# Performance work log

Hardware: AMD Instinct MI355X
Metric: run time of the kernel (lower is better)

## Reference

```python
import jax, jax.numpy as jnp
import numpy as np
from jax import lax

B, S, I, H, O, L = 32, 512, 256, 1024, 256, 3


def setup_inputs() -> dict:
    key = jax.random.key(0)
    ks = jax.random.split(key, 10)
    sc = 0.02
    return {
        "x": jax.random.normal(ks[0], (B, S, I), dtype=jnp.float32),
        "h0": jnp.zeros((B, L, H), dtype=jnp.float32),
        # layer 0 params: gates ordered [z, r, g]
        "Wx0": jax.random.normal(ks[1], (3, H, I), dtype=jnp.float32) * sc,
        "Wh0": jax.random.normal(ks[2], (3, H, H), dtype=jnp.float32) * sc,
        "bh0": jax.random.normal(ks[3], (3, H), dtype=jnp.float32) * sc,
        # layers 1..L-1 params (input dim = H)
        "Wx": jax.random.normal(ks[4], (L - 1, 3, H, H), dtype=jnp.float32) * sc,
        "Wh": jax.random.normal(ks[5], (L - 1, 3, H, H), dtype=jnp.float32) * sc,
        "bh": jax.random.normal(ks[6], (L - 1, 3, H), dtype=jnp.float32) * sc,
        "Wout": jax.random.normal(ks[7], (O, H), dtype=jnp.float32) * sc,
        "bout": jax.random.normal(ks[8], (O,), dtype=jnp.float32) * sc,
    }


def _gru_layer(x_seq, h0, Wx, Wh, bh):
    # x_seq: [S,B,Iin], h0: [B,H], Wx: [3,H,Iin], Wh: [3,H,H], bh: [3,H]
    # Precompute all input projections once (fused GEMM over full sequence).
    xproj = jnp.einsum('sbi,ghi->sbgh', x_seq, Wx)  # [S,B,3,H]

    def step(h, xp):
        z = jax.nn.sigmoid(xp[:, 0] + h @ Wh[0].T + bh[0])
        r = jax.nn.sigmoid(xp[:, 1] + h @ Wh[1].T + bh[1])
        g = jnp.tanh(xp[:, 2] + (r * h) @ Wh[2].T + bh[2])
        h_new = z * h + (1.0 - z) * g
        return h_new, h_new

    h_last, hs = lax.scan(step, h0, xproj)
    return hs, h_last  # hs: [S,B,H]


def reference(x, h0, Wx0, Wh0, bh0, Wx, Wh, bh, Wout, bout):
    seq = jnp.transpose(x, (1, 0, 2))  # [S,B,I]
    cur, hl = _gru_layer(seq, h0[:, 0], Wx0, Wh0, bh0)
    finals = [hl]
    n_extra = Wx.shape[0]
    for i in range(n_extra):  # small fixed layer count
        cur, hl = _gru_layer(cur, h0[:, i + 1], Wx[i], Wh[i], bh[i])
        finals.append(hl)
    out = cur @ Wout.T + bout  # [S,B,O]
    layer_output = jnp.transpose(out, (1, 0, 2))  # [B,S,O]
    hidden_state = jnp.stack(finals, axis=1)  # [B,L,H]
    return layer_output, hidden_state
```

## Files before the change

kernel.cpp:

```cpp
#include <hip/hip_runtime.h>
#include <cstdint>
#include <cstddef>

#define S_  512
#define H_  1024
#define H3  3072
#define OUT_OFF 4194304

typedef __attribute__((ext_vector_type(8))) short  short8;
typedef __attribute__((ext_vector_type(4))) float  f32x4;
typedef __attribute__((ext_vector_type(4))) unsigned short us4;
typedef __attribute__((ext_vector_type(4))) unsigned int   u32x4;
typedef unsigned long long u64;

#define MFMA __builtin_amdgcn_mfma_f32_16x16x32_bf16

static const size_t XP_OFF    = 0;
static const size_t H2_OFF    = 100663296;
static const size_t XBF_OFF   = 134217728;
static const size_t WX0B_OFF  = 142606336;
static const size_t WZR0_OFF  = 144179200;
static const size_t WG0_OFF   = 148373504;
static const size_t WZR1_OFF  = 150470656;
static const size_t WGX1_OFF  = 158859264;
static const size_t WG1_OFF   = 160956416;
static const size_t WZR2_OFF  = 163053568;
static const size_t WGX2_OFF  = 171442176;
static const size_t WG2_OFF   = 173539328;
static const size_t WOUTB_OFF = 175636480;
static const size_t ZBU_OFF   = 176160768;
static const size_t GXB_OFF   = 176553984;
static const size_t HROW_OFF  = 176947200;
static const size_t FLAG_OFF  = 177340416;
static const size_t HH_OFF    = 177344512;
static const size_t RHH_OFF   = 278597632;
static const size_t WS_HIST   = 379654144;
static const size_t WS_BASE   = 177737728;

__device__ inline unsigned short f2bf(float f){
  unsigned u = __builtin_bit_cast(unsigned, f);
  unsigned r = u + 0x7fffu + ((u >> 16) & 1u);
  return (unsigned short)(r >> 16);
}
__device__ inline float bf2f(unsigned short s){
  unsigned u = ((unsigned)s) << 16;
  return __builtin_bit_cast(float, u);
}
__device__ inline unsigned ld_sys(const unsigned* p){
  return __hip_atomic_load(p, __ATOMIC_RELAXED, __HIP_MEMORY_SCOPE_AGENT);
}
__device__ inline void st_sys(unsigned* p, unsigned v){
  __hip_atomic_store(p, v, __ATOMIC_RELAXED, __HIP_MEMORY_SCOPE_AGENT);
}
__device__ inline void st_rel(unsigned* p, unsigned v){
  __hip_atomic_store(p, v, __ATOMIC_RELEASE, __HIP_MEMORY_SCOPE_AGENT);
}
__device__ inline u64 ld64(const u64* p){
  return __hip_atomic_load(p, __ATOMIC_RELAXED, __HIP_MEMORY_SCOPE_AGENT);
}
__device__ inline void st64(u64* p, u64 v){
  __hip_atomic_store(p, v, __ATOMIC_RELAXED, __HIP_MEMORY_SCOPE_AGENT);
}
template<bool HIST>
__device__ inline u64 LD(const u64* p){
  if constexpr (HIST) return *p; else return ld64(p);
}
__device__ inline short8 mk8u(u64 a, u64 b){
  u32x4 u; u.x = (unsigned)a; u.y = (unsigned)(a >> 32); u.z = (unsigned)b; u.w = (unsigned)(b >> 32);
  return __builtin_bit_cast(short8, u);
}
__device__ inline u64 pk4(float a, float b, float c, float d){
  return (u64)f2bf(a) | ((u64)f2bf(b) << 16) | ((u64)f2bf(c) << 32) | ((u64)f2bf(d) << 48);
}
__device__ inline u64 pk2f(float a, float b){
  return (u64)__builtin_bit_cast(unsigned, a) | ((u64)__builtin_bit_cast(unsigned, b) << 32);
}
__device__ inline float lo32f(u64 u){ return __builtin_bit_cast(float, (unsigned)u); }
__device__ inline float hi32f(u64 u){ return __builtin_bit_cast(float, (unsigned)(u >> 32)); }

__global__ void k_conv(const float* __restrict__ src, unsigned short* __restrict__ dst, int n){
  int i = blockIdx.x*256 + threadIdx.x;
  if (i < n) dst[i] = f2bf(src[i]);
}
__global__ void k_packzr(const float* __restrict__ Wh, const float* __restrict__ Wx,
                         unsigned short* __restrict__ dst){
  size_t i = (size_t)blockIdx.x*256 + threadIdx.x;
  int k = (int)(i & 2047);
  int n = (int)(i >> 11);
  float v = (k < 1024) ? Wh[(size_t)n*1024 + k] : Wx[(size_t)n*1024 + (k - 1024)];
  dst[i] = f2bf(v);
}
__global__ void k_convx(const float* __restrict__ x, unsigned short* __restrict__ xbf){
  int row = blockIdx.x;
  int s = row >> 5, b = row & 31;
  int i = threadIdx.x;
  xbf[(size_t)row*256 + i] = f2bf(x[((size_t)b*S_ + s)*256 + i]);
}

__global__ __launch_bounds__(256) void k_gemm(const unsigned short* __restrict__ A,
                                              const unsigned short* __restrict__ Bw,
                                              const float* __restrict__ bias,
                                              void* __restrict__ Cout,
                                              int Kd, int mode, int Nd){
  __shared__ __align__(16) unsigned short lA[128*40];
  __shared__ __align__(16) unsigned short lB[128*40];
  int bm = blockIdx.y * 128, bn = blockIdx.x * 128;
  int tid = threadIdx.x;
  int w = tid >> 6, lane = tid & 63, q = lane >> 4, cc = lane & 15;
  int wm = (w >> 1) * 64, wn = (w & 1) * 64;
  f32x4 acc[4][4] = {};
  for (int k0 = 0; k0 < Kd; k0 += 32){
    #pragma unroll
    for (int i = 0; i < 2; i++){
      int idx = tid + i*256;
      int r = idx >> 2, ch = idx & 3;
      int m = bm + r;
      int arow = (mode == 0) ? m : ((m & 511)*32 + (m >> 9));
      *(u32x4*)(lA + r*40 + ch*8) = *(const u32x4*)(A + (size_t)arow*Kd + k0 + ch*8);
      *(u32x4*)(lB + r*40 + ch*8) = *(const u32x4*)(Bw + (size_t)(bn + r)*Kd + k0 + ch*8);
    }
    __syncthreads();
    short8 af[4], bfv[4];
    #pragma unroll
    for (int i = 0; i < 4; i++) af[i]  = *(const short8*)(lA + (wm + i*16 + cc)*40 + q*8);
    #pragma unroll
    for (int i = 0; i < 4; i++) bfv[i] = *(const short8*)(lB + (wn + i*16 + cc)*40 + q*8);
    #pragma unroll
    for (int i = 0; i < 4; i++)
      #pragma unroll
      for (int j = 0; j < 4; j++)
        acc[i][j] = MFMA(af[i], bfv[j], acc[i][j], 0, 0, 0);
    __syncthreads();
  }
  if (mode == 0){
    unsigned short* xp = (unsigned short*)Cout;
    #pragma unroll
    for (int i = 0; i < 4; i++){
      #pragma unroll
      for (int j = 0; j < 4; j++){
        int m = bm + wm + i*16 + q*4;
        int n = bn + wn + j*16 + cc;
        float bv = bias[n];
        int s = m >> 5, b0 = m & 31;
        us4 pk;
        #pragma unroll
        for (int reg = 0; reg < 4; reg++) pk[reg] = f2bf(acc[i][j][reg] + bv);
        *(us4*)(xp + ((size_t)s*H3 + n)*32 + b0) = pk;
      }
    }
  } else {
    float* C = (float*)Cout;
    #pragma unroll
    for (int i = 0; i < 4; i++){
      #pragma unroll
      for (int j = 0; j < 4; j++){
        int m = bm + wm + i*16 + q*4;
        int n = bn + wn + j*16 + cc;
        float bv = bias[n];
        #pragma unroll
        for (int reg = 0; reg < 4; reg++)
          C[(size_t)(m + reg)*Nd + n] = acc[i][j][reg] + bv;
      }
    }
  }
}

__device__ inline void gbar(unsigned* flags, unsigned ep){
  __syncthreads();
  if (threadIdx.x == 0) st_sys(flags + blockIdx.x, ep);
  if (threadIdx.x < 64){
    for (;;){
      unsigned v0 = ld_sys(flags + threadIdx.x);
      unsigned v1 = ld_sys(flags + 64 + threadIdx.x);
      unsigned v2 = ld_sys(flags + 128 + threadIdx.x);
      unsigned v3 = ld_sys(flags + 192 + threadIdx.x);
      if (__all((v0 >= ep) && (v1 >= ep) && (v2 >= ep) && (v3 >= ep))) break;
      __builtin_amdgcn_s_sleep(1);
    }
  }
  __syncthreads();
}

template<int NITER, bool HIST>
__device__ inline void matvec(const u64* p0, const unsigned short* wp,
                              f32x4& acc0, f32x4& acc1){
  u64 buf[2][4][4];
  #pragma unroll
  for (int ii = 0; ii < 4; ii++){
    const u64* p = p0 + ii*256;
    buf[0][ii][0] = LD<HIST>(p);      buf[0][ii][1] = LD<HIST>(p + 32);
    buf[0][ii][2] = LD<HIST>(p + 16); buf[0][ii][3] = LD<HIST>(p + 48);
  }
  constexpr int NCH = NITER / 4;
  #pragma unroll
  for (int ch = 0; ch < NCH; ch++){
    const int cur = ch & 1, nxt = cur ^ 1;
    if (ch + 1 < NCH){
      #pragma unroll
      for (int ii = 0; ii < 4; ii++){
        const u64* p = p0 + ((ch+1)*4 + ii)*256;
        buf[nxt][ii][0] = LD<HIST>(p);      buf[nxt][ii][1] = LD<HIST>(p + 32);
        buf[nxt][ii][2] = LD<HIST>(p + 16); buf[nxt][ii][3] = LD<HIST>(p + 48);
      }
    }
    #pragma unroll
    for (int ii = 0; ii < 4; ii++){
      short8 bw = *(const short8*)(wp + (ch*4 + ii)*32);
      acc0 = MFMA(mk8u(buf[cur][ii][0], buf[cur][ii][1]), bw, acc0, 0, 0, 0);
      acc1 = MFMA(mk8u(buf[cur][ii][2], buf[cur][ii][3]), bw, acc1, 0, 0, 0);
    }
  }
}

template<int MODE>
__global__ __launch_bounds__(256, 1) void k_fused(char* __restrict__ ws,
                                                  const float* __restrict__ h0,
                                                  const float* __restrict__ bh,
                                                  float* __restrict__ outp,
                                                  u64* __restrict__ hh,
                                                  u64* __restrict__ rhh){
  constexpr bool HIST = (MODE >= 1);
  constexpr bool DF   = (MODE == 2);

  __shared__ __align__(16) unsigned short wlds[65920];
  __shared__ __align__(16) float red[2][3][64][10];
  __shared__ float rtA[16*33];
  __shared__ float rtB[16*33];

  const int tid = threadIdx.x;
  const int w = tid >> 6, lane = tid & 63, q = (lane >> 4) & 3, c = lane & 15;
  const int i = blockIdx.x;

  const int lz   = 1 + (i >> 7);
  const int g2   = (i >> 6) & 1;
  const int n2   = (i & 63) << 4;
  const bool isl0 = (i < 128);
  const int g1   = (i >> 6) & 1;
  const int lgx  = 1 + ((i >> 6) & 1);
  const int n1   = (i & 63) << 4;
  const bool hasB = (i < 192);
  const int lb   = i >> 6;
  const int nb   = (i & 63) << 4;

  const unsigned short* xp = (const unsigned short*)(ws + XP_OFF);
  u64* h2u   = (u64*)(ws + H2_OFF);
  u64* zbu   = (u64*)(ws + ZBU_OFF);
  u64* gxb   = (u64*)(ws + GXB_OFF);
  float* hrow = (float*)(ws + HROW_OFF);
  unsigned* flags = (unsigned*)(ws + FLAG_OFF);
  unsigned* fA2 = flags;
  unsigned* fA0 = flags + 256;
  unsigned* fA1 = flags + 512;
  unsigned* fB0 = flags + 768;

  int catA = (lane < 32) ? 0 : ((lane < 48) ? 1 : 2);
  int idxA = 0;
  if (lane < 32)      idxA = 64*((w < 2) ? lz : (lz-1)) + (w & 1)*32 + lane;
  else if (lane < 48) idxA = 64*(isl0 ? 0 : (lgx-1)) + w*16 + (lane - 32);
  else if (lane == 48){
    if (w == 0){ idxA = 64*lz + (i & 63); catA = 0; }
    else if (w == 1){ idxA = (isl0 ? 0 : 64*lgx) + (i & 63); catA = 1; }
  }
  const unsigned* pollA = fB0 + idxA;
  const unsigned* pollB = fA0;
  bool reqB_lane = false;
  if (hasB){
    if (lane < 16){
      pollB = (lb == 0) ? (fA2 + 16*w + lane)
                        : (fA0 + ((lb == 1) ? 64 : 192) + 16*w + lane);
      reqB_lane = true;
    } else if (w == 0 && lane == 16){
      pollB = (lb == 0) ? (fA1 + (i & 63))
            : (lb == 1) ? (fA0 + (i & 63))
                        : (fA0 + 128 + (i & 63));
      reqB_lane = true;
    } else if (w == 0 && lane == 17 && lb >= 1){
      pollB = (lb == 1) ? (fA1 + 128 + (i & 63)) : (fA1 + 192 + (i & 63));
      reqB_lane = true;
    }
  }

  {
    const unsigned short* src2 = (const unsigned short*)(ws + (lz == 1 ? WZR1_OFF : WZR2_OFF))
                                 + (size_t)(g2*1024 + n2)*2048;
    for (int idx = tid; idx < 4096; idx += 256){
      int kc = idx & 255, row = idx >> 8;
      u32x4 v = *(const u32x4*)(src2 + (size_t)row*2048 + kc*8);
      *(u32x4*)(wlds + row*2056 + kc*8) = v;
    }
    const unsigned short* src1 = isl0
      ? (const unsigned short*)(ws + WZR0_OFF) + (size_t)(g1*1024 + n1)*1024
      : (const unsigned short*)(ws + (lgx == 1 ? WGX1_OFF : WGX2_OFF)) + (size_t)n1*1024;
    for (int idx = tid; idx < 2048; idx += 256){
      int kc = idx & 127, row = idx >> 7;
      u32x4 v = *(const u32x4*)(src1 + (size_t)row*1024 + kc*8);
      *(u32x4*)(wlds + 32896 + row*1032 + kc*8) = v;
    }
    if (hasB){
      const unsigned short* srcb = (const unsigned short*)(ws + (lb == 0 ? WG0_OFF : (lb == 1 ? WG1_OFF : WG2_OFF)))
                                   + (size_t)nb*1024;
      for (int idx = tid; idx < 2048; idx += 256){
        int kc = idx & 127, row = idx >> 7;
        u32x4 v = *(const u32x4*)(srcb + (size_t)row*1024 + kc*8);
        *(u32x4*)(wlds + 49408 + row*1032 + kc*8) = v;
      }
    }
  }
  const float biasT2 = bh[(size_t)(lz-1)*H3 + g2*1024 + n2 + c];
  const float biasGX = isl0 ? 0.f : bh[(size_t)(lgx-1)*H3 + 2048 + n1 + c];

  if (hasB){
    for (int idx = tid; idx < 512; idx += 256){
      int n = idx >> 5, b = idx & 31;
      float v = h0[((size_t)b*3 + lb)*H_ + nb + n];
      hrow[((size_t)lb*1024 + nb + n)*32 + b] = v;
      rtA[n*33 + b] = v;
    }
  }
  __syncthreads();
  if (hasB && tid < 64){
    int b = tid & 31, p2b = (tid >> 5)*2;
    #pragma unroll
    for (int pp = 0; pp < 2; pp++){
      int p2 = p2b + pp;
      u64 pkv = pk4(rtA[(4*p2+0)*33+b], rtA[(4*p2+1)*33+b], rtA[(4*p2+2)*33+b], rtA[(4*p2+3)*33+b]);
      st64(hh + (size_t)(HIST ? lb : 0)*24576 + (size_t)lb*8192 + (size_t)((nb >> 2) + p2)*32 + b, pkv);
    }
  }
  unsigned ep = 1;
  if constexpr (DF){
    if (tid == 0 && hasB) st_rel(fB0 + i, (unsigned)(lb + 1));
    __syncthreads();
  } else {
    gbar(flags, ep); ep++;
  }

  for (int T = 0; T < 514; T++){
    const int t2 = T - lz;
    const bool actT2 = (unsigned)t2 < 512u;
    const int t1 = isl0 ? T : (T - lgx);
    const bool actT1 = (unsigned)t1 < 512u;
    const int tb = T - lb;
    const bool actB = hasB && ((unsigned)tb < 512u);

    const u64* hslotR = hh + (size_t)(HIST ? T : 0)*24576;
    u64*       rslot  = rhh + (size_t)(HIST ? T : 0)*24576;

    if constexpr (DF){
      const bool req = (catA == 0) ? actT2 : ((catA == 1) ? actT1 : false);
      const unsigned epw = (unsigned)(T + 1);
      for (;;){
        unsigned v = req ? ld_sys(pollA) : 0xFFFFFFFFu;
        if (__all(v >= epw)) break;
      }
    }

    u64 hpreA[8]; us4 xpreA[2]; u64 hpreL0[8];
    if (actT2 && w == 0 && g2 == 1){
      const u64* hb = hslotR + (size_t)lz*8192 + (size_t)((n2 + c) >> 2)*32 + q*4;
      #pragma unroll
      for (int mt = 0; mt < 2; mt++)
        #pragma unroll
        for (int r = 0; r < 4; r++) hpreA[mt*4+r] = LD<HIST>(hb + mt*16 + r);
    }
    if (actT1 && w == 1 && isl0){
      const unsigned short* xr = xp + ((size_t)t1*H3 + g1*1024 + n1 + c)*32 + q*4;
      xpreA[0] = *(const us4*)(xr);
      xpreA[1] = *(const us4*)(xr + 16);
      if (g1 == 1){
        const u64* hb = hslotR + (size_t)((n1 + c) >> 2)*32 + q*4;
        #pragma unroll
        for (int mt = 0; mt < 2; mt++)
          #pragma unroll
          for (int r = 0; r < 4; r++) hpreL0[mt*4+r] = LD<HIST>(hb + mt*16 + r);
      }
    }

    f32x4 z20 = {0,0,0,0}, z21 = {0,0,0,0};
    f32x4 z10 = {0,0,0,0}, z11 = {0,0,0,0};
    if (actT2){
      const u64* p0 = hslotR + (size_t)((w < 2) ? lz : (lz-1))*8192 + (size_t)((w & 1)*128 + q*2)*32 + c;
      const unsigned short* wp = wlds + c*2056 + w*512 + q*8;
      matvec<16, HIST>(p0, wp, z20, z21);
    }
    if (actT1){
      const u64* p0 = hslotR + (size_t)(isl0 ? 0 : (lgx-1))*8192 + (size_t)(w*64 + q*2)*32 + c;
      const unsigned short* wp = wlds + 32896 + c*1032 + w*256 + q*8;
      matvec<8, HIST>(p0, wp, z10, z11);
    }
    if (actT2 && w > 0){
      float* p = &red[0][w-1][lane][0];
      #pragma unroll
      for (int r = 0; r < 4; r++){ p[r] = z20[r]; p[4+r] = z21[r]; }
    }
    if (actT1 && w != 1){
      float* p = &red[1][(w == 0) ? 0 : (w-1)][lane][0];
      #pragma unroll
      for (int r = 0; r < 4; r++){ p[r] = z10[r]; p[4+r] = z11[r]; }
    }
    __syncthreads();
    if (w == 0 && actT2){
      #pragma unroll
      for (int s = 0; s < 3; s++){
        const float* p = &red[0][s][lane][0];
        #pragma unroll
        for (int r = 0; r < 4; r++){ z20[r] += p[r]; z21[r] += p[4+r]; }
      }
      const int sh = (c & 3)*16;
      #pragma unroll
      for (int mt = 0; mt < 2; mt++){
        float f[4];
        #pragma unroll
        for (int r = 0; r < 4; r++){
          float pre = (mt ? z21[r] : z20[r]) + biasT2;
          f[r] = 1.0f / (1.0f + __expf(-pre));
        }
        if (g2 == 0){
          u64* zp = zbu + ((size_t)lz*1024 + n2 + c)*16 + mt*8 + q*2;
          st64(zp, pk2f(f[0], f[1])); st64(zp + 1, pk2f(f[2], f[3]));
        } else {
          #pragma unroll
          for (int r = 0; r < 4; r++){
            int b = mt*16 + q*4 + r;
            rtA[c*33 + b] = f[r] * bf2f((unsigned short)(hpreA[mt*4+r] >> sh));
          }
        }
      }
      if constexpr (DF){
        if (g2 == 0 && lane == 0) st_rel(fA0 + i, (unsigned)(T + 1));
      }
    }
    if (w == 1 && actT1){
      #pragma unroll
      for (int s = 0; s < 3; s++){
        const float* p = &red[1][s][lane][0];
        #pragma unroll
        for (int r = 0; r < 4; r++){ z10[r] += p[r]; z11[r] += p[4+r]; }
      }
      if (isl0){
        const int sh = (c & 3)*16;
        #pragma unroll
        for (int mt = 0; mt < 2; mt++){
          us4 xv = xpreA[mt];
          float f[4];
          #pragma unroll
          for (int r = 0; r < 4; r++){
            float pre = (mt ? z11[r] : z10[r]) + bf2f(xv[r]);
            f[r] = 1.0f / (1.0f + __expf(-pre));
          }
          if (g1 == 0){
            u64* zp = zbu + ((size_t)n1 + c)*16 + mt*8 + q*2;
            st64(zp, pk2f(f[0], f[1])); st64(zp + 1, pk2f(f[2], f[3]));
          } else {
            #pragma unroll
            for (int r = 0; r < 4; r++){
              int b = mt*16 + q*4 + r;
              rtB[c*33 + b] = f[r] * bf2f((unsigned short)(hpreL0[mt*4+r] >> sh));
            }
          }
        }
        if constexpr (DF){
          if (g1 == 0 && lane == 0) st_rel(fA1 + i, (unsigned)(T + 1));
        }
      } else {
        #pragma unroll
        for (int mt = 0; mt < 2; mt++){
          float f[4];
          #pragma unroll
          for (int r = 0; r < 4; r++) f[r] = (mt ? z11[r] : z10[r]) + biasGX;
          u64* gp = gxb + ((size_t)lgx*1024 + n1 + c)*16 + mt*8 + q*2;
          st64(gp, pk2f(f[0], f[1])); st64(gp + 1, pk2f(f[2], f[3]));
        }
        if constexpr (DF){
          if (lane == 0) st_rel(fA1 + i, (unsigned)(T + 1));
        }
      }
    }
    __syncthreads();
    if (g2 == 1 && actT2 && tid < 64){
      int b = tid & 31, p2b = (tid >> 5)*2;
      #pragma unroll
      for (int pp = 0; pp < 2; pp++){
        int p2 = p2b + pp;
        st64(rslot + (size_t)lz*8192 + (size_t)((n2 >> 2) + p2)*32 + b,
             pk4(rtA[(4*p2+0)*33+b], rtA[(4*p2+1)*33+b], rtA[(4*p2+2)*33+b], rtA[(4*p2+3)*33+b]));
      }
      if constexpr (DF){
        if (tid == 0) st_rel(fA0 + i, (unsigned)(T + 1));
      }
    }
    if (isl0 && g1 == 1 && actT1 && tid >= 128 && tid < 192){
      int tt = tid - 128; int b = tt & 31, p2b = (tt >> 5)*2;
      #pragma unroll
      for (int pp = 0; pp < 2; pp++){
        int p2 = p2b + pp;
        st64(rslot + (size_t)((n1 >> 2) + p2)*32 + b,
             pk4(rtB[(4*p2+0)*33+b], rtB[(4*p2+1)*33+b], rtB[(4*p2+2)*33+b], rtB[(4*p2+3)*33+b]));
      }
      if constexpr (DF){
        if (tid == 128) st_rel(fA2 + (i - 64), (unsigned)(T + 1));
      }
    }
    if constexpr (DF){
      const unsigned epw = (unsigned)(T + 1);
      const bool req = reqB_lane && actB;
      for (;;){
        unsigned v = req ? ld_sys(pollB) : 0xFFFFFFFFu;
        if (__all(v >= epw)) break;
      }
    } else {
      gbar(flags, ep); ep++;
    }

    u64 zpreB[4], gpreB[4]; us4 xpreB[2]; f32x4 hpre4[2];
    if (actB && w == 0){
      const u64* zp = zbu + ((size_t)lb*1024 + nb + c)*16 + q*2;
      zpreB[0] = ld64(zp);     zpreB[1] = ld64(zp + 1);
      zpreB[2] = ld64(zp + 8); zpreB[3] = ld64(zp + 9);
      if (lb == 0){
        const unsigned short* xr = xp + ((size_t)tb*H3 + 2048 + nb + c)*32 + q*4;
        xpreB[0] = *(const us4*)(xr);
        xpreB[1] = *(const us4*)(xr + 16);
      } else {
        const u64* gp = gxb + ((size_t)lb*1024 + nb + c)*16 + q*2;
        gpreB[0] = ld64(gp);     gpreB[1] = ld64(gp + 1);
        gpreB[2] = ld64(gp + 8); gpreB[3] = ld64(gp + 9);
      }
      const float* hp0 = hrow + ((size_t)lb*1024 + nb + c)*32 + q*4;
      hpre4[0] = *(const f32x4*)(hp0);
      hpre4[1] = *(const f32x4*)(hp0 + 16);
    }

    f32x4 gb0 = {0,0,0,0}, gb1 = {0,0,0,0};
    if (actB){
      const u64* p0 = (const u64*)rslot + (size_t)lb*8192 + (size_t)(w*64 + q*2)*32 + c;
      const unsigned short* wp = wlds + 49408 + c*1032 + w*256 + q*8;
      matvec<8, HIST>(p0, wp, gb0, gb1);
      if (w > 0){
        float* p = &red[0][w-1][lane][0];
        #pragma unroll
        for (int r = 0; r < 4; r++){ p[r] = gb0[r]; p[4+r] = gb1[r]; }
      }
    }
    __syncthreads();
    if (actB && w == 0){
      #pragma unroll
      for (int s = 0; s < 3; s++){
        const float* p = &red[0][s][lane][0];
        #pragma unroll
        for (int r = 0; r < 4; r++){ gb0[r] += p[r]; gb1[r] += p[4+r]; }
      }
      #pragma unroll
      for (int mt = 0; mt < 2; mt++){
        float gadd[4];
        if (lb == 0){
          us4 xv = xpreB[mt];
          #pragma unroll
          for (int r = 0; r < 4; r++) gadd[r] = bf2f(xv[r]);
        } else {
          gadd[0] = lo32f(gpreB[mt*2]);   gadd[1] = hi32f(gpreB[mt*2]);
          gadd[2] = lo32f(gpreB[mt*2+1]); gadd[3] = hi32f(gpreB[mt*2+1]);
        }
        float zf[4] = { lo32f(zpreB[mt*2]),   hi32f(zpreB[mt*2]),
                        lo32f(zpreB[mt*2+1]), hi32f(zpreB[mt*2+1]) };
        f32x4 h4 = hpre4[mt];
        f32x4 hn4;
        #pragma unroll
        for (int r = 0; r < 4; r++){
          float gpre = (mt ? gb1[r] : gb0[r]) + gadd[r];
          float gv = tanhf(gpre);
          float hnv = zf[r]*h4[r] + (1.0f - zf[r])*gv;
          hn4[r] = hnv;
          rtA[c*33 + mt*16 + q*4 + r] = hnv;
          if (tb == 511) outp[OUT_OFF + ((size_t)(mt*16 + q*4 + r)*3 + lb)*H_ + nb + c] = hnv;
        }
        *(f32x4*)(hrow + ((size_t)lb*1024 + nb + c)*32 + mt*16 + q*4) = hn4;
      }
    }
    if (actB && tid < 64){
      int b = tid & 31, p2b = (tid >> 5)*2;
      #pragma unroll
      for (int pp = 0; pp < 2; pp++){
        int p2 = p2b + pp;
        u64 pkv = pk4(rtA[(4*p2+0)*33+b], rtA[(4*p2+1)*33+b], rtA[(4*p2+2)*33+b], rtA[(4*p2+3)*33+b]);
        st64(hh + (size_t)(HIST ? (T + 1) : 0)*24576 + (size_t)lb*8192 + (size_t)((nb >> 2) + p2)*32 + b, pkv);
        if (lb == 2) *(u64*)(h2u + ((size_t)tb*32 + b)*256 + (nb >> 2) + p2) = pkv;
      }
    }
    if constexpr (DF){
      if (actB && tid == 0) st_rel(fB0 + i, (unsigned)(T + 2));
      __syncthreads();
    } else {
      gbar(flags, ep); ep++;
    }
  }
  (void)ep;
}

extern "C" void kernel_launch(void* const* d_in, const int* in_sizes, int n_in,
                              void* d_out, int out_size, void* d_ws, size_t ws_size,
                              hipStream_t stream){
  (void)in_sizes; (void)n_in; (void)out_size;
  if (ws_size < WS_BASE) return;
  const bool hist = (ws_size >= WS_HIST);

  const float* x    = (const float*)d_in[0];
  const float* h0   = (const float*)d_in[1];
  const float* Wx0  = (const float*)d_in[2];
  const float* Wh0  = (const float*)d_in[3];
  const float* bh0  = (const float*)d_in[4];
  const float* Wx   = (const float*)d_in[5];
  const float* Wh   = (const float*)d_in[6];
  const float* bh   = (const float*)d_in[7];
  const float* Wout = (const float*)d_in[8];
  const float* bout = (const float*)d_in[9];
  float* out = (float*)d_out;

  char* ws = (char*)d_ws;
  unsigned short* xp    = (unsigned short*)(ws + XP_OFF);
  unsigned short* h2    = (unsigned short*)(ws + H2_OFF);
  unsigned short* xbf   = (unsigned short*)(ws + XBF_OFF);
  unsigned short* wx0b  = (unsigned short*)(ws + WX0B_OFF);
  unsigned short* wzr0  = (unsigned short*)(ws + WZR0_OFF);
  unsigned short* wg0   = (unsigned short*)(ws + WG0_OFF);
  unsigned short* wzr1  = (unsigned short*)(ws + WZR1_OFF);
  unsigned short* wgx1  = (unsigned short*)(ws + WGX1_OFF);
  unsigned short* wg1   = (unsigned short*)(ws + WG1_OFF);
  unsigned short* wzr2  = (unsigned short*)(ws + WZR2_OFF);
  unsigned short* wgx2  = (unsigned short*)(ws + WGX2_OFF);
  unsigned short* wg2   = (unsigned short*)(ws + WG2_OFF);
  unsigned short* woutb = (unsigned short*)(ws + WOUTB_OFF);
  u64* hh  = (u64*)(ws + HH_OFF);
  u64* rhh = hist ? (u64*)(ws + RHH_OFF) : (hh + 24576);

  hipMemsetAsync(ws + FLAG_OFF, 0, 4096, stream);

  k_conv<<<3072, 256, 0, stream>>>(Wx0, wx0b, 786432);
  k_conv<<<8192, 256, 0, stream>>>(Wh0, wzr0, 2097152);
  k_conv<<<4096, 256, 0, stream>>>(Wh0 + 2097152, wg0, 1048576);
  k_packzr<<<16384, 256, 0, stream>>>(Wh, Wx, wzr1);
  k_conv<<<4096, 256, 0, stream>>>(Wx + 2097152, wgx1, 1048576);
  k_conv<<<4096, 256, 0, stream>>>(Wh + 2097152, wg1, 1048576);
  k_packzr<<<16384, 256, 0, stream>>>(Wh + 3145728, Wx + 3145728, wzr2);
  k_conv<<<4096, 256, 0, stream>>>(Wx + 5242880, wgx2, 1048576);
  k_conv<<<4096, 256, 0, stream>>>(Wh + 5242880, wg2, 1048576);
  k_conv<<<1024, 256, 0, stream>>>(Wout, woutb, 262144);
  k_convx<<<16384, 256, 0, stream>>>(x, xbf);

  {
    dim3 g(24, 128);
    k_gemm<<<g, 256, 0, stream>>>(xbf, wx0b, bh0, (void*)xp, 256, 0, H3);
  }
  if (hist) k_fused<2><<<256, 256, 0, stream>>>(ws, h0, bh, out, hh, rhh);
  else      k_fused<0><<<256, 256, 0, stream>>>(ws, h0, bh, out, hh, rhh);
  {
    dim3 g(2, 128);
    k_gemm<<<g, 256, 0, stream>>>(h2, woutb, bout, (void*)out, 1024, 1, 256);
  }
}
```

Baseline: 7.189 ms.

## Replace block barriers with wave-local LDS fences for rslot and hh publishing

The wave that computes the r*h or new-h tile now packs and publishes it to global memory itself, after a wave-local LDS wait, instead of waiting at a block-wide __syncthreads and handing the work to tid<64. Two __syncthreads per step are removed, and a separate reduction buffer redB is added so phase B does not alias phase A's buffer once the barrier is gone. This targets per-timestep latency on the serial critical path of the recurrent pipeline. It relies on intra-wave LDS ordering holding and on the extra buffer fitting in LDS.

```diff
diff --git a/kernel.cpp b/kernel.cpp
--- a/kernel.cpp
+++ b/kernel.cpp
@@ -77,6 +77,10 @@
 }
 __device__ inline float lo32f(u64 u){ return __builtin_bit_cast(float, (unsigned)u); }
 __device__ inline float hi32f(u64 u){ return __builtin_bit_cast(float, (unsigned)(u >> 32)); }
+__device__ inline void lds_wave_fence(){
+  __asm__ __volatile__("s_waitcnt lgkmcnt(0)" ::: "memory");
+  __builtin_amdgcn_sched_barrier(0);
+}
 
 __global__ void k_conv(const float* __restrict__ src, unsigned short* __restrict__ dst, int n){
   int i = blockIdx.x*256 + threadIdx.x;
@@ -224,6 +228,7 @@
 
   __shared__ __align__(16) unsigned short wlds[65920];
   __shared__ __align__(16) float red[2][3][64][10];
+  __shared__ __align__(16) float redB[3][64][10];
   __shared__ float rtA[16*33];
   __shared__ float rtB[16*33];
 
@@ -426,8 +431,18 @@
           }
         }
       }
-      if constexpr (DF){
-        if (g2 == 0 && lane == 0) st_rel(fA0 + i, (unsigned)(T + 1));
+      if (g2 == 0){
+        if constexpr (DF){ if (lane == 0) st_rel(fA0 + i, (unsigned)(T + 1)); }
+      } else {
+        lds_wave_fence();
+        int b = lane & 31, p2b = (lane >> 5)*2;
+        #pragma unroll
+        for (int pp = 0; pp < 2; pp++){
+          int p2 = p2b + pp;
+          st64(rslot + (size_t)lz*8192 + (size_t)((n2 >> 2) + p2)*32 + b,
+               pk4(rtA[(4*p2+0)*33+b], rtA[(4*p2+1)*33+b], rtA[(4*p2+2)*33+b], rtA[(4*p2+3)*33+b]));
+        }
+        if constexpr (DF){ if (lane == 0) st_rel(fA0 + i, (unsigned)(T + 1)); }
       }
     }
     if (w == 1 && actT1){
@@ -459,8 +474,18 @@
             }
           }
         }
-        if constexpr (DF){
-          if (g1 == 0 && lane == 0) st_rel(fA1 + i, (unsigned)(T + 1));
+        if (g1 == 0){
+          if constexpr (DF){ if (lane == 0) st_rel(fA1 + i, (unsigned)(T + 1)); }
+        } else {
+          lds_wave_fence();
+          int b = lane & 31, p2b = (lane >> 5)*2;
+          #pragma unroll
+          for (int pp = 0; pp < 2; pp++){
+            int p2 = p2b + pp;
+            st64(rslot + (size_t)((n1 >> 2) + p2)*32 + b,
+                 pk4(rtB[(4*p2+0)*33+b], rtB[(4*p2+1)*33+b], rtB[(4*p2+2)*33+b], rtB[(4*p2+3)*33+b]));
+          }
+          if constexpr (DF){ if (lane == 0) st_rel(fA2 + (i - 64), (unsigned)(T + 1)); }
         }
       } else {
         #pragma unroll
@@ -471,34 +496,7 @@
           u64* gp = gxb + ((size_t)lgx*1024 + n1 + c)*16 + mt*8 + q*2;
           st64(gp, pk2f(f[0], f[1])); st64(gp + 1, pk2f(f[2], f[3]));
         }
-        if constexpr (DF){
-          if (lane == 0) st_rel(fA1 + i, (unsigned)(T + 1));
-        }
-      }
-    }
-    __syncthreads();
-    if (g2 == 1 && actT2 && tid < 64){
-      int b = tid & 31, p2b = (tid >> 5)*2;
-      #pragma unroll
-      for (int pp = 0; pp < 2; pp++){
-        int p2 = p2b + pp;
-        st64(rslot + (size_t)lz*8192 + (size_t)((n2 >> 2) + p2)*32 + b,
-             pk4(rtA[(4*p2+0)*33+b], rtA[(4*p2+1)*33+b], rtA[(4*p2+2)*33+b], rtA[(4*p2+3)*33+b]));
-      }
-      if constexpr (DF){
-        if (tid == 0) st_rel(fA0 + i, (unsigned)(T + 1));
-      }
-    }
-    if (isl0 && g1 == 1 && actT1 && tid >= 128 && tid < 192){
-      int tt = tid - 128; int b = tt & 31, p2b = (tt >> 5)*2;
-      #pragma unroll
-      for (int pp = 0; pp < 2; pp++){
-        int p2 = p2b + pp;
-        st64(rslot + (size_t)((n1 >> 2) + p2)*32 + b,
-             pk4(rtB[(4*p2+0)*33+b], rtB[(4*p2+1)*33+b], rtB[(4*p2+2)*33+b], rtB[(4*p2+3)*33+b]));
-      }
-      if constexpr (DF){
-        if (tid == 128) st_rel(fA2 + (i - 64), (unsigned)(T + 1));
+        if constexpr (DF){ if (lane == 0) st_rel(fA1 + i, (unsigned)(T + 1)); }
       }
     }
     if constexpr (DF){
@@ -537,7 +535,7 @@
       const unsigned short* wp = wlds + 49408 + c*1032 + w*256 + q*8;
       matvec<8, HIST>(p0, wp, gb0, gb1);
       if (w > 0){
-        float* p = &red[0][w-1][lane][0];
+        float* p = &redB[w-1][lane][0];
         #pragma unroll
         for (int r = 0; r < 4; r++){ p[r] = gb0[r]; p[4+r] = gb1[r]; }
       }
@@ -546,7 +544,7 @@
     if (actB && w == 0){
       #pragma unroll
       for (int s = 0; s < 3; s++){
-        const float* p = &red[0][s][lane][0];
+        const float* p = &redB[s][lane][0];
         #pragma unroll
         for (int r = 0; r < 4; r++){ gb0[r] += p[r]; gb1[r] += p[4+r]; }
       }
@@ -576,9 +574,8 @@
         }
         *(f32x4*)(hrow + ((size_t)lb*1024 + nb + c)*32 + mt*16 + q*4) = hn4;
       }
-    }
-    if (actB && tid < 64){
-      int b = tid & 31, p2b = (tid >> 5)*2;
+      lds_wave_fence();
+      int b = lane & 31, p2b = (lane >> 5)*2;
       #pragma unroll
       for (int pp = 0; pp < 2; pp++){
         int p2 = p2b + pp;
@@ -586,11 +583,11 @@
         st64(hh + (size_t)(HIST ? (T + 1) : 0)*24576 + (size_t)lb*8192 + (size_t)((nb >> 2) + p2)*32 + b, pkv);
         if (lb == 2) *(u64*)(h2u + ((size_t)tb*32 + b)*256 + (nb >> 2) + p2) = pkv;
       }
-    }
-    if constexpr (DF){
-      if (actB && tid == 0) st_rel(fB0 + i, (unsigned)(T + 2));
-      __syncthreads();
-    } else {
+      if constexpr (DF){
+        if (lane == 0) st_rel(fB0 + i, (unsigned)(T + 2));
+      }
+    }
+    if constexpr (!DF){
       gbar(flags, ep); ep++;
     }
   }
```

Result: slower. 7.497 ms (+4.3%).
